# Kernel tuning notes

Measured on AMD Instinct MI355X. Metric: run time of the kernel, lower is better.

Reference implementation:

```python
import jax, jax.numpy as jnp
import numpy as np

N, H, W, C = 8, 64, 64, 256  # C//4 = 64 query channels, HW = 4096 attention size


def setup_inputs() -> dict:
    key = jax.random.key(0)
    k1, k2, k3, k4 = jax.random.split(key, 4)
    src_mask = jax.random.uniform(k1, (N, H, W), dtype=jnp.float32)
    src_feature = jax.random.normal(k2, (N, H, W, C), dtype=jnp.float32)
    ref_feature = jax.random.normal(k3, (N, H, W, C), dtype=jnp.float32)
    w_query = jax.random.normal(k4, (C, C // 4), dtype=jnp.float32) * 0.02  # 1x1 conv weight
    return {"src_mask": src_mask, "src_feature": src_feature,
            "ref_feature": ref_feature, "w_query": w_query}


def _apply_attention_map(att_map, features):
    n, h, w, c = features.shape
    pixels = features.reshape(n, h * w, c).transpose(0, 2, 1)  # (N, C, HW)
    att_out = jnp.einsum('ncp,npq->ncq', pixels, att_map)      # (N, C, HW)
    return att_out.reshape(n, h, w, c)


def reference(src_mask, src_feature, ref_feature, w_query):
    n, h, w, c = src_feature.shape
    # 1x1 conv (no bias): per-pixel channel projection C -> C//4
    query = jnp.einsum('nhwc,cd->nhwd', src_feature, w_query).reshape(n, h * w, -1)
    # full (HW x HW) attention map, softmax over keys
    att_map = jax.nn.softmax(jnp.einsum('npd,nqd->npq', query, query), axis=-1)
    # original module applies the map to src_feature twice (src_att and ref_att)
    att_out = _apply_attention_map(att_map, src_feature)
    src_att = att_out
    ref_att = att_out
    m = src_mask[..., None]  # (N, H, W, 1)
    ex_guide_flow = m * ref_att + (1.0 - m) * ref_feature
    return jnp.concatenate([ex_guide_flow, src_att], axis=-1)  # (N, H, W, 2C)
```

## Files before the change

### kernel.cpp

```cpp
#include <hip/hip_runtime.h>

typedef unsigned short u16;
typedef unsigned int u32;
typedef __attribute__((ext_vector_type(8))) __bf16 bf16x8;
typedef __attribute__((ext_vector_type(8))) _Float16 f16x8;
typedef __attribute__((ext_vector_type(4))) float f32x4;

__device__ __forceinline__ float b2f(u16 b) {
    union { u32 u; float f; } v; v.u = ((u32)b) << 16; return v.f;
}
__device__ __forceinline__ u16 f2bf(float f) {
    union { float f; u32 u; } v; v.f = f;
    u32 u = v.u;
    return (u16)((u + 0x7fffu + ((u >> 16) & 1u)) >> 16);
}
__device__ __forceinline__ u16 f2h(float f) {
    _Float16 h = (_Float16)f;
    return __builtin_bit_cast(u16, h);
}
__device__ __forceinline__ bf16x8 ldg8b(const u16* p) {
    uint4 v = *(const uint4*)p;
    return __builtin_bit_cast(bf16x8, v);
}
__device__ __forceinline__ f16x8 ldg8h(const u16* p) {
    uint4 v = *(const uint4*)p;
    return __builtin_bit_cast(f16x8, v);
}
__device__ __forceinline__ f32x4 mfma_bf(bf16x8 a, bf16x8 b, f32x4 c) {
    return __builtin_amdgcn_mfma_f32_16x16x32_bf16(a, b, c, 0, 0, 0);
}
__device__ __forceinline__ f32x4 mfma_h(f16x8 a, f16x8 b, f32x4 c) {
    return __builtin_amdgcn_mfma_f32_16x16x32_f16(a, b, c, 0, 0, 0);
}
__device__ __forceinline__ void gld16(const u16* g, u16* l) {
    __builtin_amdgcn_global_load_lds(
        (const __attribute__((address_space(1))) u32*)g,
        (__attribute__((address_space(3))) u32*)l, 16, 0, 0);
}


__global__ void k0_wt(const float* __restrict__ Wq,
                      u16* __restrict__ Wthi, u16* __restrict__ Wtlo) {
    int idx = blockIdx.x * 256 + threadIdx.x;
    int c = idx >> 6, d = idx & 63;
    float w = Wq[idx];
    u16 hi = f2bf(w);
    float rem = w - b2f(hi);
    Wthi[d * 256 + c] = hi;
    Wtlo[d * 256 + c] = f2bf(rem);
}

__global__ __launch_bounds__(256) void k1_query(
    const float* __restrict__ F, const u16* __restrict__ Wthi,
    const u16* __restrict__ Wtlo, u16* __restrict__ Qh) {
    const int t = threadIdx.x;
    const int w = t >> 6, L = t & 63, lane16 = L & 15, quad = L >> 4;
    const int R0 = blockIdx.x * 64;
    const int row = R0 + w * 16 + lane16;
    const f32x4 z4 = {0.f, 0.f, 0.f, 0.f};
    f32x4 acc[4] = {z4, z4, z4, z4};
    union U8 { bf16x8 v; u16 s[8]; };
#pragma unroll
    for (int ks = 0; ks < 8; ++ks) {
        const float* fp = F + (size_t)row * 256 + ks * 32 + quad * 8;
        float4 x0 = *(const float4*)fp;
        float4 x1 = *(const float4*)(fp + 4);
        float xs[8] = {x0.x, x0.y, x0.z, x0.w, x1.x, x1.y, x1.z, x1.w};
        U8 ahi, alo;
#pragma unroll
        for (int j = 0; j < 8; ++j) {
            u16 h = f2bf(xs[j]);
            ahi.s[j] = h;
            alo.s[j] = f2bf(xs[j] - b2f(h));
        }
#pragma unroll
        for (int nt = 0; nt < 4; ++nt) {
            const int off = (nt * 16 + lane16) * 256 + ks * 32 + quad * 8;
            bf16x8 bh = ldg8b(Wthi + off);
            bf16x8 bl = ldg8b(Wtlo + off);
            acc[nt] = mfma_bf(ahi.v, bh, acc[nt]);
            acc[nt] = mfma_bf(alo.v, bh, acc[nt]);
            acc[nt] = mfma_bf(ahi.v, bl, acc[nt]);
        }
    }
    const int orow = R0 + w * 16 + quad * 4;
#pragma unroll
    for (int nt = 0; nt < 4; ++nt) {
        const int d = nt * 16 + lane16;
#pragma unroll
        for (int r = 0; r < 4; ++r) {
            const int p = orow + r;
            Qh[(size_t)p * 64 + (d ^ ((p & 7) << 3))] = f2h(acc[nt][r]);
        }
    }
}

__global__ __launch_bounds__(256) void k2_suminv(
    const u16* __restrict__ Q, float* __restrict__ inv_l) {
    const int t = threadIdx.x;
    const int w = t >> 6, L = t & 63, lane16 = L & 15, quad = L >> 4, l7 = lane16 & 7;
    const int bx = blockIdx.x;
    const int n = bx & 7, pb = bx >> 3;
    const int P0 = pb * 32;
    const u16* Qn = Q + (size_t)n * 4096 * 64;

    f16x8 ap[2][2];
#pragma unroll
    for (int st = 0; st < 2; ++st) {
        const int row = P0 + st * 16 + lane16;
        ap[st][0] = ldg8h(Qn + row * 64 + ((quad * 8) ^ (l7 * 8)));
        ap[st][1] = ldg8h(Qn + row * 64 + ((32 + quad * 8) ^ (l7 * 8)));
    }
    float sums[2][4];
#pragma unroll
    for (int st = 0; st < 2; ++st)
#pragma unroll
        for (int r = 0; r < 4; ++r) sums[st][r] = 0.f;

    const f32x4 z4 = {0.f, 0.f, 0.f, 0.f};
    for (int s = 0; s < 32; ++s) {
#pragma unroll
        for (int nt = 0; nt < 2; ++nt) {
            const int qr = w * 1024 + s * 32 + nt * 16 + lane16;
            f16x8 b0 = ldg8h(Qn + qr * 64 + ((quad * 8) ^ (l7 * 8)));
            f16x8 b1 = ldg8h(Qn + qr * 64 + ((32 + quad * 8) ^ (l7 * 8)));
#pragma unroll
            for (int st = 0; st < 2; ++st) {
                f32x4 z = z4;
                z = mfma_h(ap[st][0], b0, z);
                z = mfma_h(ap[st][1], b1, z);
                sums[st][0] += __expf(z[0]);
                sums[st][1] += __expf(z[1]);
                sums[st][2] += __expf(z[2]);
                sums[st][3] += __expf(z[3]);
            }
        }
    }
    __shared__ float red[4][32];
#pragma unroll
    for (int st = 0; st < 2; ++st)
#pragma unroll
        for (int r = 0; r < 4; ++r) {
            float v = sums[st][r];
            v += __shfl_xor(v, 1);
            v += __shfl_xor(v, 2);
            v += __shfl_xor(v, 4);
            v += __shfl_xor(v, 8);
            if (lane16 == 0) red[w][st * 16 + quad * 4 + r] = v;
        }
    __syncthreads();
    if (t < 32) {
        float tot = red[0][t] + red[1][t] + red[2][t] + red[3][t];
        inv_l[n * 4096 + P0 + t] = 1.0f / tot;
    }
}

__global__ __launch_bounds__(256) void k3_gt(
    const float* __restrict__ F, u16* __restrict__ Gt) {
    const int t = threadIdx.x;
    const int bx = blockIdx.x;
    const int n = bx >> 6, s = bx & 63;
    const int p0 = s * 64;
    __shared__ float tile[64][65];
    const float* Fn = F + (size_t)n * 4096 * 256;
    u16* Gn = Gt + (size_t)(n * 64 + s) * 16384;
#pragma unroll 1
    for (int ct = 0; ct < 4; ++ct) {
        const int c0 = ct * 64;
        if (ct > 0) __syncthreads();
#pragma unroll
        for (int k = 0; k < 16; ++k) {
            int idx = k * 256 + t;
            int r = idx >> 6, cc = idx & 63;
            tile[r][cc] = Fn[(size_t)(p0 + r) * 256 + c0 + cc];
        }
        __syncthreads();
#pragma unroll
        for (int k = 0; k < 2; ++k) {
            int u = k * 256 + t;
            int cc = u & 63, S = u >> 6;
            int G = S ^ (cc & 7);
            u16 v[8];
#pragma unroll
            for (int j = 0; j < 8; ++j) v[j] = f2bf(tile[G * 8 + j][cc]);
            uint4 pk;
            pk.x = (u32)v[0] | ((u32)v[1] << 16);
            pk.y = (u32)v[2] | ((u32)v[3] << 16);
            pk.z = (u32)v[4] | ((u32)v[5] << 16);
            pk.w = (u32)v[6] | ((u32)v[7] << 16);
            *(uint4*)&Gn[(c0 + cc) * 64 + S * 8] = pk;
        }
    }
}

__global__ __launch_bounds__(256, 2) void k4_attn(
    const u16* __restrict__ Q, const u16* __restrict__ Gt,
    const float* __restrict__ invl, const float* __restrict__ mask,
    const float* __restrict__ ref, float* __restrict__ out) {
    const int t = threadIdx.x;
    const int w = t >> 6, L = t & 63, lane16 = L & 15, quad = L >> 4, l7 = lane16 & 7;
    const int bx = blockIdx.x;
    const int n = bx & 7, qb = bx >> 3;
    const int q0 = qb << 6;

    __shared__ u16 sGt[16384];
    __shared__ u16 sQp[4096];
    __shared__ u16 sP[4096];

    const u16* Qn = Q + (size_t)n * 4096 * 64;
    const u16* Gtn = Gt + (size_t)n * 64 * 16384;
    const float* iln = invl + n * 4096;

    f16x8 bq[4][2];
#pragma unroll
    for (int qt = 0; qt < 4; ++qt) {
        const int row = q0 + qt * 16 + lane16;
        bq[qt][0] = ldg8h(Qn + row * 64 + ((quad * 8) ^ (l7 * 8)));
        bq[qt][1] = ldg8h(Qn + row * 64 + ((32 + quad * 8) ^ (l7 * 8)));
    }

    const int pl = w * 16 + lane16;
    const int sA0 = pl * 64 + ((quad * 8) ^ (l7 * 8));
    const int sA1 = pl * 64 + ((32 + quad * 8) ^ (l7 * 8));
    int wrP[4];
#pragma unroll
    for (int qt = 0; qt < 4; ++qt)
        wrP[qt] = (qt * 16 + lane16) * 64 +
                  ((w * 16 + 8 * (quad >> 1)) ^ (l7 * 8)) + 4 * (quad & 1);
    const int dl = L * 8;

    const f32x4 z4 = {0.f, 0.f, 0.f, 0.f};
    f32x4 acc[4][4];
#pragma unroll
    for (int a = 0; a < 4; ++a)
#pragma unroll
        for (int b = 0; b < 4; ++b) acc[a][b] = z4;

#pragma unroll
    for (int j = 0; j < 2; ++j) {
        const int c = w * 2 + j;
        gld16(Qn + c * 512 + dl, &sQp[c * 512]);
    }
    __syncthreads();

#pragma unroll 1
    for (int i = 0; i < 64; ++i) {
#pragma unroll
        for (int j = 0; j < 8; ++j) {
            const int c = w * 8 + j;
            gld16(Gtn + (size_t)i * 16384 + c * 512 + dl, &sGt[c * 512]);
        }
        {
            f16x8 a0 = ldg8h(&sQp[sA0]);
            f16x8 a1 = ldg8h(&sQp[sA1]);
            float4 il4 = *(const float4*)(iln + i * 64 + w * 16 + quad * 4);
#pragma unroll
            for (int qt = 0; qt < 4; ++qt) {
                f32x4 z = z4;
                z = mfma_h(a0, bq[qt][0], z);
                z = mfma_h(a1, bq[qt][1], z);
                ushort4 pk;
                pk.x = f2bf(__expf(z[0]) * il4.x);
                pk.y = f2bf(__expf(z[1]) * il4.y);
                pk.z = f2bf(__expf(z[2]) * il4.z);
                pk.w = f2bf(__expf(z[3]) * il4.w);
                *(ushort4*)&sP[wrP[qt]] = pk;
            }
        }
        __syncthreads();
        if (i + 1 < 64) {
#pragma unroll
            for (int j = 0; j < 2; ++j) {
                const int c = w * 2 + j;
                gld16(Qn + (size_t)(i + 1) * 4096 + c * 512 + dl, &sQp[c * 512]);
            }
        }
#pragma unroll
        for (int h = 0; h < 2; ++h) {
            bf16x8 af[4], bb[4];
#pragma unroll
            for (int m = 0; m < 4; ++m)
                af[m] = ldg8b(&sP[(m * 16 + lane16) * 64 + ((h * 32 + quad * 8) ^ (l7 * 8))]);
#pragma unroll
            for (int nt = 0; nt < 4; ++nt)
                bb[nt] = ldg8b(&sGt[(w * 64 + nt * 16 + lane16) * 64 +
                                    ((h * 32 + quad * 8) ^ (l7 * 8))]);
#pragma unroll
            for (int nt = 0; nt < 4; ++nt)
#pragma unroll
                for (int m = 0; m < 4; ++m)
                    acc[m][nt] = mfma_bf(af[m], bb[nt], acc[m][nt]);
        }
        __syncthreads();
    }

    const int tb = qb >> 2;
    const int cb = (qb & 3) * 64;
    const float* maskn = mask + n * 4096;
    const float* refn = ref + (size_t)n * 4096 * 256;
    float* outn = out + (size_t)n * 4096 * 512;
#pragma unroll
    for (int nt = 0; nt < 4; ++nt) {
        const int ch = w * 64 + nt * 16 + lane16;
        const int pixel = ch * 16 + tb;
        const float m = maskn[pixel];
#pragma unroll
        for (int mt = 0; mt < 4; ++mt) {
            const int c4 = cb + mt * 16 + quad * 4;
            float4 r4 = *(const float4*)(refn + (size_t)pixel * 256 + c4);
            float a0 = acc[mt][nt][0], a1 = acc[mt][nt][1];
            float a2 = acc[mt][nt][2], a3 = acc[mt][nt][3];
            float4 a4 = {a0, a1, a2, a3};
            float4 bl4 = {m * a0 + (1.f - m) * r4.x,
                          m * a1 + (1.f - m) * r4.y,
                          m * a2 + (1.f - m) * r4.z,
                          m * a3 + (1.f - m) * r4.w};
            *(float4*)(outn + (size_t)pixel * 512 + 256 + c4) = a4;
            *(float4*)(outn + (size_t)pixel * 512 + c4) = bl4;
        }
    }
}

extern "C" void kernel_launch(void* const* d_in, const int* in_sizes, int n_in,
                              void* d_out, int out_size, void* d_ws, size_t ws_size,
                              hipStream_t stream) {
    const float* mask = (const float*)d_in[0];
    const float* F    = (const float*)d_in[1];
    const float* ref  = (const float*)d_in[2];
    const float* Wq   = (const float*)d_in[3];
    float* out = (float*)d_out;
    char* ws = (char*)d_ws;

    u16*   Wthi = (u16*)ws;
    u16*   Wtlo = (u16*)(ws + 32768);
    u16*   Qh   = (u16*)(ws + 65536);
    float* invl = (float*)(ws + 65536 + 4194304);
    u16*   Gt   = (u16*)(ws + 65536 + 4194304 + 131072);

    k0_wt    <<<64,   256, 0, stream>>>(Wq, Wthi, Wtlo);
    k1_query <<<512,  256, 0, stream>>>(F, Wthi, Wtlo, Qh);
    k2_suminv<<<1024, 256, 0, stream>>>(Qh, invl);
    k3_gt    <<<512,  256, 0, stream>>>(F, Gt);
    k4_attn  <<<512,  256, 0, stream>>>(Qh, Gt, invl, mask, ref, out);
}
```

Baseline: 271.7 us.

## Double-buffer P tile, read Gt and Q directly from global, fold normalizer into exp2

The attention kernel no longer stages the Gt value tile and Q slice in LDS through async global-to-LDS loads. MFMA operands are now read straight from global memory, and the P tile is double-buffered so the next step's softmax probabilities are computed while the current step's product runs, leaving one barrier per iteration instead of two. The row-sum kernel now stores -log2(sum), and each probability becomes exp2(z*log2e + lg), replacing an exp and a multiply with an fma and an exp2, with packed bf16 conversion. The risk is that Gt is re-read from global/L2 by every wave instead of being shared through LDS, adding memory traffic and latency.

```diff
diff --git a/kernel.cpp b/kernel.cpp
--- a/kernel.cpp
+++ b/kernel.cpp
@@ -18,6 +18,11 @@
     _Float16 h = (_Float16)f;
     return __builtin_bit_cast(u16, h);
 }
+__device__ __forceinline__ u32 pkbf2(float a, float b) {
+    u16 x = __builtin_bit_cast(u16, (__bf16)a);
+    u16 y = __builtin_bit_cast(u16, (__bf16)b);
+    return (u32)x | ((u32)y << 16);
+}
 __device__ __forceinline__ bf16x8 ldg8b(const u16* p) {
     uint4 v = *(const uint4*)p;
     return __builtin_bit_cast(bf16x8, v);
@@ -32,11 +37,8 @@
 __device__ __forceinline__ f32x4 mfma_h(f16x8 a, f16x8 b, f32x4 c) {
     return __builtin_amdgcn_mfma_f32_16x16x32_f16(a, b, c, 0, 0, 0);
 }
-__device__ __forceinline__ void gld16(const u16* g, u16* l) {
-    __builtin_amdgcn_global_load_lds(
-        (const __attribute__((address_space(1))) u32*)g,
-        (__attribute__((address_space(3))) u32*)l, 16, 0, 0);
-}
+
+#define LOG2E 1.44269504088896340736f
 
 
 __global__ void k0_wt(const float* __restrict__ Wq,
@@ -96,7 +98,7 @@
 }
 
 __global__ __launch_bounds__(256) void k2_suminv(
-    const u16* __restrict__ Q, float* __restrict__ inv_l) {
+    const u16* __restrict__ Q, float* __restrict__ lgl) {
     const int t = threadIdx.x;
     const int w = t >> 6, L = t & 63, lane16 = L & 15, quad = L >> 4, l7 = lane16 & 7;
     const int bx = blockIdx.x;
@@ -151,7 +153,7 @@
     __syncthreads();
     if (t < 32) {
         float tot = red[0][t] + red[1][t] + red[2][t] + red[3][t];
-        inv_l[n * 4096 + P0 + t] = 1.0f / tot;
+        lgl[n * 4096 + P0 + t] = -__log2f(tot);
     }
 }
 
@@ -195,7 +197,7 @@
 
 __global__ __launch_bounds__(256, 2) void k4_attn(
     const u16* __restrict__ Q, const u16* __restrict__ Gt,
-    const float* __restrict__ invl, const float* __restrict__ mask,
+    const float* __restrict__ lgl, const float* __restrict__ mask,
     const float* __restrict__ ref, float* __restrict__ out) {
     const int t = threadIdx.x;
     const int w = t >> 6, L = t & 63, lane16 = L & 15, quad = L >> 4, l7 = lane16 & 7;
@@ -203,13 +205,11 @@
     const int n = bx & 7, qb = bx >> 3;
     const int q0 = qb << 6;
 
-    __shared__ u16 sGt[16384];
-    __shared__ u16 sQp[4096];
-    __shared__ u16 sP[4096];
+    __shared__ u16 sP[2][4096];
 
     const u16* Qn = Q + (size_t)n * 4096 * 64;
     const u16* Gtn = Gt + (size_t)n * 64 * 16384;
-    const float* iln = invl + n * 4096;
+    const float* iln = lgl + n * 4096;
 
     f16x8 bq[4][2];
 #pragma unroll
@@ -219,15 +219,24 @@
         bq[qt][1] = ldg8h(Qn + row * 64 + ((32 + quad * 8) ^ (l7 * 8)));
     }
 
-    const int pl = w * 16 + lane16;
-    const int sA0 = pl * 64 + ((quad * 8) ^ (l7 * 8));
-    const int sA1 = pl * 64 + ((32 + quad * 8) ^ (l7 * 8));
+    const int sAg0 = (w * 16 + lane16) * 64 + ((quad * 8) ^ (l7 * 8));
+    const int sAg1 = (w * 16 + lane16) * 64 + ((32 + quad * 8) ^ (l7 * 8));
     int wrP[4];
 #pragma unroll
     for (int qt = 0; qt < 4; ++qt)
         wrP[qt] = (qt * 16 + lane16) * 64 +
                   ((w * 16 + 8 * (quad >> 1)) ^ (l7 * 8)) + 4 * (quad & 1);
-    const int dl = L * 8;
+    int rdP[4][2], gOf[4][2];
+#pragma unroll
+    for (int m = 0; m < 4; ++m)
+#pragma unroll
+        for (int h = 0; h < 2; ++h)
+            rdP[m][h] = (m * 16 + lane16) * 64 + ((h * 32 + quad * 8) ^ (l7 * 8));
+#pragma unroll
+    for (int nt = 0; nt < 4; ++nt)
+#pragma unroll
+        for (int h = 0; h < 2; ++h)
+            gOf[nt][h] = (w * 64 + nt * 16 + lane16) * 64 + ((h * 32 + quad * 8) ^ (l7 * 8));
 
     const f32x4 z4 = {0.f, 0.f, 0.f, 0.f};
     f32x4 acc[4][4];
@@ -236,60 +245,61 @@
 #pragma unroll
         for (int b = 0; b < 4; ++b) acc[a][b] = z4;
 
-#pragma unroll
-    for (int j = 0; j < 2; ++j) {
-        const int c = w * 2 + j;
-        gld16(Qn + c * 512 + dl, &sQp[c * 512]);
+    {
+        f16x8 a0 = ldg8h(Qn + sAg0);
+        f16x8 a1 = ldg8h(Qn + sAg1);
+        float4 il4 = *(const float4*)(iln + w * 16 + quad * 4);
+        float lg[4] = {il4.x, il4.y, il4.z, il4.w};
+#pragma unroll
+        for (int qt = 0; qt < 4; ++qt) {
+            f32x4 z = z4;
+            z = mfma_h(a0, bq[qt][0], z);
+            z = mfma_h(a1, bq[qt][1], z);
+            uint2 pk;
+            pk.x = pkbf2(__builtin_exp2f(__builtin_fmaf(z[0], LOG2E, lg[0])),
+                         __builtin_exp2f(__builtin_fmaf(z[1], LOG2E, lg[1])));
+            pk.y = pkbf2(__builtin_exp2f(__builtin_fmaf(z[2], LOG2E, lg[2])),
+                         __builtin_exp2f(__builtin_fmaf(z[3], LOG2E, lg[3])));
+            *(uint2*)&sP[0][wrP[qt]] = pk;
+        }
     }
     __syncthreads();
 
 #pragma unroll 1
     for (int i = 0; i < 64; ++i) {
-#pragma unroll
-        for (int j = 0; j < 8; ++j) {
-            const int c = w * 8 + j;
-            gld16(Gtn + (size_t)i * 16384 + c * 512 + dl, &sGt[c * 512]);
-        }
-        {
-            f16x8 a0 = ldg8h(&sQp[sA0]);
-            f16x8 a1 = ldg8h(&sQp[sA1]);
-            float4 il4 = *(const float4*)(iln + i * 64 + w * 16 + quad * 4);
+        const u16* sPc = &sP[i & 1][0];
+        u16* sPn = &sP[(i + 1) & 1][0];
+        const u16* gstep = Gtn + (size_t)i * 16384;
+#pragma unroll
+        for (int h = 0; h < 2; ++h) {
+            bf16x8 af[4], bb[4];
+#pragma unroll
+            for (int m = 0; m < 4; ++m) af[m] = ldg8b(&sPc[rdP[m][h]]);
+#pragma unroll
+            for (int nt = 0; nt < 4; ++nt) bb[nt] = ldg8b(gstep + gOf[nt][h]);
+#pragma unroll
+            for (int nt = 0; nt < 4; ++nt)
+#pragma unroll
+                for (int m = 0; m < 4; ++m)
+                    acc[m][nt] = mfma_bf(af[m], bb[nt], acc[m][nt]);
+        }
+        if (i + 1 < 64) {
+            f16x8 a0 = ldg8h(Qn + (i + 1) * 4096 + sAg0);
+            f16x8 a1 = ldg8h(Qn + (i + 1) * 4096 + sAg1);
+            float4 il4 = *(const float4*)(iln + (i + 1) * 64 + w * 16 + quad * 4);
+            float lg[4] = {il4.x, il4.y, il4.z, il4.w};
 #pragma unroll
             for (int qt = 0; qt < 4; ++qt) {
                 f32x4 z = z4;
                 z = mfma_h(a0, bq[qt][0], z);
                 z = mfma_h(a1, bq[qt][1], z);
-                ushort4 pk;
-                pk.x = f2bf(__expf(z[0]) * il4.x);
-                pk.y = f2bf(__expf(z[1]) * il4.y);
-                pk.z = f2bf(__expf(z[2]) * il4.z);
-                pk.w = f2bf(__expf(z[3]) * il4.w);
-                *(ushort4*)&sP[wrP[qt]] = pk;
+                uint2 pk;
+                pk.x = pkbf2(__builtin_exp2f(__builtin_fmaf(z[0], LOG2E, lg[0])),
+                             __builtin_exp2f(__builtin_fmaf(z[1], LOG2E, lg[1])));
+                pk.y = pkbf2(__builtin_exp2f(__builtin_fmaf(z[2], LOG2E, lg[2])),
+                             __builtin_exp2f(__builtin_fmaf(z[3], LOG2E, lg[3])));
+                *(uint2*)&sPn[wrP[qt]] = pk;
             }
-        }
-        __syncthreads();
-        if (i + 1 < 64) {
-#pragma unroll
-            for (int j = 0; j < 2; ++j) {
-                const int c = w * 2 + j;
-                gld16(Qn + (size_t)(i + 1) * 4096 + c * 512 + dl, &sQp[c * 512]);
-            }
-        }
-#pragma unroll
-        for (int h = 0; h < 2; ++h) {
-            bf16x8 af[4], bb[4];
-#pragma unroll
-            for (int m = 0; m < 4; ++m)
-                af[m] = ldg8b(&sP[(m * 16 + lane16) * 64 + ((h * 32 + quad * 8) ^ (l7 * 8))]);
-#pragma unroll
-            for (int nt = 0; nt < 4; ++nt)
-                bb[nt] = ldg8b(&sGt[(w * 64 + nt * 16 + lane16) * 64 +
-                                    ((h * 32 + quad * 8) ^ (l7 * 8))]);
-#pragma unroll
-            for (int nt = 0; nt < 4; ++nt)
-#pragma unroll
-                for (int m = 0; m < 4; ++m)
-                    acc[m][nt] = mfma_bf(af[m], bb[nt], acc[m][nt]);
         }
         __syncthreads();
     }
@@ -334,12 +344,12 @@
     u16*   Wthi = (u16*)ws;
     u16*   Wtlo = (u16*)(ws + 32768);
     u16*   Qh   = (u16*)(ws + 65536);
-    float* invl = (float*)(ws + 65536 + 4194304);
+    float* lgl  = (float*)(ws + 65536 + 4194304);
     u16*   Gt   = (u16*)(ws + 65536 + 4194304 + 131072);
 
     k0_wt    <<<64,   256, 0, stream>>>(Wq, Wthi, Wtlo);
     k1_query <<<512,  256, 0, stream>>>(F, Wthi, Wtlo, Qh);
-    k2_suminv<<<1024, 256, 0, stream>>>(Qh, invl);
+    k2_suminv<<<1024, 256, 0, stream>>>(Qh, lgl);
     k3_gt    <<<512,  256, 0, stream>>>(F, Gt);
-    k4_attn  <<<512,  256, 0, stream>>>(Qh, Gt, invl, mask, ref, out);
-}
+    k4_attn  <<<512,  256, 0, stream>>>(Qh, Gt, lgl, mask, ref, out);
+}
```

Measured after the change: 335.5 us. +23.5%, slower.

## Use 8 waves in attention kernel, fold normalizer into exp2, use hardware bf16 conversion

Applied to the files above, without the earlier changes.

The attention kernel now launches 512 threads per block (8 waves), halving per-wave channel tiles and query tiles so each wave holds fewer accumulators. The aim is to raise occupancy and hide the latency of the LDS and global loads. The row-sum kernel now stores -log2 of the sum, so the probability becomes a single fma plus exp2 instead of exp and a multiply. Float-to-bf16 conversion now uses the compiler's native __bf16 cast, which can map to a packed hardware convert. More waves share each barrier, so synchronization costs more, and the pre-scaled exp2 form may change rounding slightly.

```diff
diff --git a/kernel.cpp b/kernel.cpp
--- a/kernel.cpp
+++ b/kernel.cpp
@@ -10,13 +10,16 @@
     union { u32 u; float f; } v; v.u = ((u32)b) << 16; return v.f;
 }
 __device__ __forceinline__ u16 f2bf(float f) {
-    union { float f; u32 u; } v; v.f = f;
-    u32 u = v.u;
-    return (u16)((u + 0x7fffu + ((u >> 16) & 1u)) >> 16);
+    return __builtin_bit_cast(u16, (__bf16)f);
 }
 __device__ __forceinline__ u16 f2h(float f) {
     _Float16 h = (_Float16)f;
     return __builtin_bit_cast(u16, h);
+}
+__device__ __forceinline__ u32 pkbf2(float a, float b) {
+    u16 x = __builtin_bit_cast(u16, (__bf16)a);
+    u16 y = __builtin_bit_cast(u16, (__bf16)b);
+    return (u32)x | ((u32)y << 16);
 }
 __device__ __forceinline__ bf16x8 ldg8b(const u16* p) {
     uint4 v = *(const uint4*)p;
@@ -37,6 +40,8 @@
         (const __attribute__((address_space(1))) u32*)g,
         (__attribute__((address_space(3))) u32*)l, 16, 0, 0);
 }
+
+#define LOG2E 1.44269504088896340736f
 
 
 __global__ void k0_wt(const float* __restrict__ Wq,
@@ -96,7 +101,7 @@
 }
 
 __global__ __launch_bounds__(256) void k2_suminv(
-    const u16* __restrict__ Q, float* __restrict__ inv_l) {
+    const u16* __restrict__ Q, float* __restrict__ lgl) {
     const int t = threadIdx.x;
     const int w = t >> 6, L = t & 63, lane16 = L & 15, quad = L >> 4, l7 = lane16 & 7;
     const int bx = blockIdx.x;
@@ -151,7 +156,7 @@
     __syncthreads();
     if (t < 32) {
         float tot = red[0][t] + red[1][t] + red[2][t] + red[3][t];
-        inv_l[n * 4096 + P0 + t] = 1.0f / tot;
+        lgl[n * 4096 + P0 + t] = -__log2f(tot);
     }
 }
 
@@ -180,28 +185,27 @@
             int u = k * 256 + t;
             int cc = u & 63, S = u >> 6;
             int G = S ^ (cc & 7);
-            u16 v[8];
-#pragma unroll
-            for (int j = 0; j < 8; ++j) v[j] = f2bf(tile[G * 8 + j][cc]);
             uint4 pk;
-            pk.x = (u32)v[0] | ((u32)v[1] << 16);
-            pk.y = (u32)v[2] | ((u32)v[3] << 16);
-            pk.z = (u32)v[4] | ((u32)v[5] << 16);
-            pk.w = (u32)v[6] | ((u32)v[7] << 16);
+            pk.x = pkbf2(tile[G * 8 + 0][cc], tile[G * 8 + 1][cc]);
+            pk.y = pkbf2(tile[G * 8 + 2][cc], tile[G * 8 + 3][cc]);
+            pk.z = pkbf2(tile[G * 8 + 4][cc], tile[G * 8 + 5][cc]);
+            pk.w = pkbf2(tile[G * 8 + 6][cc], tile[G * 8 + 7][cc]);
             *(uint4*)&Gn[(c0 + cc) * 64 + S * 8] = pk;
         }
     }
 }
 
-__global__ __launch_bounds__(256, 2) void k4_attn(
+__global__ __launch_bounds__(512, 4) void k4_attn(
     const u16* __restrict__ Q, const u16* __restrict__ Gt,
-    const float* __restrict__ invl, const float* __restrict__ mask,
+    const float* __restrict__ lgl, const float* __restrict__ mask,
     const float* __restrict__ ref, float* __restrict__ out) {
     const int t = threadIdx.x;
     const int w = t >> 6, L = t & 63, lane16 = L & 15, quad = L >> 4, l7 = lane16 & 7;
     const int bx = blockIdx.x;
     const int n = bx & 7, qb = bx >> 3;
     const int q0 = qb << 6;
+    const int ps = w & 3;
+    const int qh = w >> 2;
 
     __shared__ u16 sGt[16384];
     __shared__ u16 sQp[4096];
@@ -209,84 +213,77 @@
 
     const u16* Qn = Q + (size_t)n * 4096 * 64;
     const u16* Gtn = Gt + (size_t)n * 64 * 16384;
-    const float* iln = invl + n * 4096;
-
-    f16x8 bq[4][2];
-#pragma unroll
-    for (int qt = 0; qt < 4; ++qt) {
-        const int row = q0 + qt * 16 + lane16;
+    const float* iln = lgl + n * 4096;
+
+    f16x8 bq[2][2];
+#pragma unroll
+    for (int qt = 0; qt < 2; ++qt) {
+        const int row = q0 + qh * 32 + qt * 16 + lane16;
         bq[qt][0] = ldg8h(Qn + row * 64 + ((quad * 8) ^ (l7 * 8)));
         bq[qt][1] = ldg8h(Qn + row * 64 + ((32 + quad * 8) ^ (l7 * 8)));
     }
 
-    const int pl = w * 16 + lane16;
+    const int pl = ps * 16 + lane16;
     const int sA0 = pl * 64 + ((quad * 8) ^ (l7 * 8));
     const int sA1 = pl * 64 + ((32 + quad * 8) ^ (l7 * 8));
-    int wrP[4];
-#pragma unroll
-    for (int qt = 0; qt < 4; ++qt)
-        wrP[qt] = (qt * 16 + lane16) * 64 +
-                  ((w * 16 + 8 * (quad >> 1)) ^ (l7 * 8)) + 4 * (quad & 1);
+    int wrP[2];
+#pragma unroll
+    for (int qt = 0; qt < 2; ++qt)
+        wrP[qt] = (qh * 32 + qt * 16 + lane16) * 64 +
+                  ((ps * 16 + 8 * (quad >> 1)) ^ (l7 * 8)) + 4 * (quad & 1);
     const int dl = L * 8;
 
     const f32x4 z4 = {0.f, 0.f, 0.f, 0.f};
-    f32x4 acc[4][4];
+    f32x4 acc[4][2];
 #pragma unroll
     for (int a = 0; a < 4; ++a)
 #pragma unroll
-        for (int b = 0; b < 4; ++b) acc[a][b] = z4;
-
-#pragma unroll
-    for (int j = 0; j < 2; ++j) {
-        const int c = w * 2 + j;
-        gld16(Qn + c * 512 + dl, &sQp[c * 512]);
-    }
+        for (int b = 0; b < 2; ++b) acc[a][b] = z4;
+
+    gld16(Qn + w * 512 + dl, &sQp[w * 512]);
     __syncthreads();
 
 #pragma unroll 1
     for (int i = 0; i < 64; ++i) {
 #pragma unroll
-        for (int j = 0; j < 8; ++j) {
-            const int c = w * 8 + j;
+        for (int j = 0; j < 4; ++j) {
+            const int c = w * 4 + j;
             gld16(Gtn + (size_t)i * 16384 + c * 512 + dl, &sGt[c * 512]);
         }
         {
             f16x8 a0 = ldg8h(&sQp[sA0]);
             f16x8 a1 = ldg8h(&sQp[sA1]);
-            float4 il4 = *(const float4*)(iln + i * 64 + w * 16 + quad * 4);
-#pragma unroll
-            for (int qt = 0; qt < 4; ++qt) {
+            float4 il4 = *(const float4*)(iln + i * 64 + ps * 16 + quad * 4);
+            float lg0 = il4.x, lg1 = il4.y, lg2 = il4.z, lg3 = il4.w;
+#pragma unroll
+            for (int qt = 0; qt < 2; ++qt) {
                 f32x4 z = z4;
                 z = mfma_h(a0, bq[qt][0], z);
                 z = mfma_h(a1, bq[qt][1], z);
-                ushort4 pk;
-                pk.x = f2bf(__expf(z[0]) * il4.x);
-                pk.y = f2bf(__expf(z[1]) * il4.y);
-                pk.z = f2bf(__expf(z[2]) * il4.z);
-                pk.w = f2bf(__expf(z[3]) * il4.w);
-                *(ushort4*)&sP[wrP[qt]] = pk;
+                uint2 pk;
+                pk.x = pkbf2(__builtin_exp2f(__builtin_fmaf(z[0], LOG2E, lg0)),
+                             __builtin_exp2f(__builtin_fmaf(z[1], LOG2E, lg1)));
+                pk.y = pkbf2(__builtin_exp2f(__builtin_fmaf(z[2], LOG2E, lg2)),
+                             __builtin_exp2f(__builtin_fmaf(z[3], LOG2E, lg3)));
+                *(uint2*)&sP[wrP[qt]] = pk;
             }
         }
         __syncthreads();
         if (i + 1 < 64) {
-#pragma unroll
-            for (int j = 0; j < 2; ++j) {
-                const int c = w * 2 + j;
-                gld16(Qn + (size_t)(i + 1) * 4096 + c * 512 + dl, &sQp[c * 512]);
-            }
+            gld16(Qn + (size_t)(i + 1) * 4096 + w * 512 + dl, &sQp[w * 512]);
         }
 #pragma unroll
         for (int h = 0; h < 2; ++h) {
-            bf16x8 af[4], bb[4];
+            bf16x8 af[4], bb[2];
 #pragma unroll
             for (int m = 0; m < 4; ++m)
                 af[m] = ldg8b(&sP[(m * 16 + lane16) * 64 + ((h * 32 + quad * 8) ^ (l7 * 8))]);
 #pragma unroll
-            for (int nt = 0; nt < 4; ++nt)
-                bb[nt] = ldg8b(&sGt[(w * 64 + nt * 16 + lane16) * 64 +
+            for (int nt = 0; nt < 2; ++nt)
+                bb[nt] = ldg8b(&sGt[(w * 32 + nt * 16 + lane16) * 64 +
                                     ((h * 32 + quad * 8) ^ (l7 * 8))]);
 #pragma unroll
-            for (int nt = 0; nt < 4; ++nt)
+            for (int nt = 0; nt < 2; ++nt)
 #pragma unroll
                 for (int m = 0; m < 4; ++m)
                     acc[m][nt] = mfma_bf(af[m], bb[nt], acc[m][nt]);
@@ -300,8 +297,8 @@
     const float* refn = ref + (size_t)n * 4096 * 256;
     float* outn = out + (size_t)n * 4096 * 512;
 #pragma unroll
-    for (int nt = 0; nt < 4; ++nt) {
-        const int ch = w * 64 + nt * 16 + lane16;
+    for (int nt = 0; nt < 2; ++nt) {
+        const int ch = w * 32 + nt * 16 + lane16;
         const int pixel = ch * 16 + tb;
         const float m = maskn[pixel];
 #pragma unroll
@@ -334,12 +331,12 @@
     u16*   Wthi = (u16*)ws;
     u16*   Wtlo = (u16*)(ws + 32768);
     u16*   Qh   = (u16*)(ws + 65536);
-    float* invl = (float*)(ws + 65536 + 4194304);
+    float* lgl  = (float*)(ws + 65536 + 4194304);
     u16*   Gt   = (u16*)(ws + 65536 + 4194304 + 131072);
 
     k0_wt    <<<64,   256, 0, stream>>>(Wq, Wthi, Wtlo);
     k1_query <<<512,  256, 0, stream>>>(F, Wthi, Wtlo, Qh);
-    k2_suminv<<<1024, 256, 0, stream>>>(Qh, invl);
+    k2_suminv<<<1024, 256, 0, stream>>>(Qh, lgl);
     k3_gt    <<<512,  256, 0, stream>>>(F, Gt);
-    k4_attn  <<<512,  256, 0, stream>>>(Qh, Gt, invl, mask, ref, out);
-}
+    k4_attn  <<<512,  512, 0, stream>>>(Qh, Gt, lgl, mask, ref, out);
+}
```

New measurement: 294.9 us. 8.6% more time.

## Fuse query projection and bf16 transpose of features into one kernel

Applied to the files above, without the earlier changes.

Merges the query projection kernel and the feature transpose/convert kernel so the fp32 feature tile is read from global memory once into LDS and reused for both the Gt layout write and the split-bf16 MFMA projection. This removes one full pass over the 32 MB feature tensor and one kernel launch. It also swaps the manual rounding in the transpose path for native bf16 conversion, and pads the tile to 68 columns so the float4 reads from LDS are aligned, which may add bank conflicts on the column-wise transpose reads.

```diff
diff --git a/kernel.cpp b/kernel.cpp
--- a/kernel.cpp
+++ b/kernel.cpp
@@ -17,6 +17,11 @@
 __device__ __forceinline__ u16 f2h(float f) {
     _Float16 h = (_Float16)f;
     return __builtin_bit_cast(u16, h);
+}
+__device__ __forceinline__ u32 pkbf2(float a, float b) {
+    u16 x = __builtin_bit_cast(u16, (__bf16)a);
+    u16 y = __builtin_bit_cast(u16, (__bf16)b);
+    return (u32)x | ((u32)y << 16);
 }
 __device__ __forceinline__ bf16x8 ldg8b(const u16* p) {
     uint4 v = *(const uint4*)p;
@@ -50,37 +55,70 @@
     Wtlo[d * 256 + c] = f2bf(rem);
 }
 
-__global__ __launch_bounds__(256) void k1_query(
+__global__ __launch_bounds__(256) void k13_query_gt(
     const float* __restrict__ F, const u16* __restrict__ Wthi,
-    const u16* __restrict__ Wtlo, u16* __restrict__ Qh) {
+    const u16* __restrict__ Wtlo, u16* __restrict__ Qh,
+    u16* __restrict__ Gt) {
     const int t = threadIdx.x;
     const int w = t >> 6, L = t & 63, lane16 = L & 15, quad = L >> 4;
-    const int R0 = blockIdx.x * 64;
-    const int row = R0 + w * 16 + lane16;
+    const int bx = blockIdx.x;
+    const int R0 = bx * 64;
+    const int n = bx >> 6, s = bx & 63;
+
+    __shared__ float tile[64][68];
+    const float* Fn = F + (size_t)R0 * 256;
+    u16* Gn = Gt + (size_t)(n * 64 + s) * 16384;
+
     const f32x4 z4 = {0.f, 0.f, 0.f, 0.f};
     f32x4 acc[4] = {z4, z4, z4, z4};
     union U8 { bf16x8 v; u16 s[8]; };
-#pragma unroll
-    for (int ks = 0; ks < 8; ++ks) {
-        const float* fp = F + (size_t)row * 256 + ks * 32 + quad * 8;
-        float4 x0 = *(const float4*)fp;
-        float4 x1 = *(const float4*)(fp + 4);
-        float xs[8] = {x0.x, x0.y, x0.z, x0.w, x1.x, x1.y, x1.z, x1.w};
-        U8 ahi, alo;
-#pragma unroll
-        for (int j = 0; j < 8; ++j) {
-            u16 h = f2bf(xs[j]);
-            ahi.s[j] = h;
-            alo.s[j] = f2bf(xs[j] - b2f(h));
-        }
-#pragma unroll
-        for (int nt = 0; nt < 4; ++nt) {
-            const int off = (nt * 16 + lane16) * 256 + ks * 32 + quad * 8;
-            bf16x8 bh = ldg8b(Wthi + off);
-            bf16x8 bl = ldg8b(Wtlo + off);
-            acc[nt] = mfma_bf(ahi.v, bh, acc[nt]);
-            acc[nt] = mfma_bf(alo.v, bh, acc[nt]);
-            acc[nt] = mfma_bf(ahi.v, bl, acc[nt]);
+
+#pragma unroll 1
+    for (int ct = 0; ct < 4; ++ct) {
+        const int c0 = ct * 64;
+        if (ct > 0) __syncthreads();
+#pragma unroll
+        for (int k = 0; k < 16; ++k) {
+            int idx = k * 256 + t;
+            int r = idx >> 6, cc = idx & 63;
+            tile[r][cc] = Fn[(size_t)r * 256 + c0 + cc];
+        }
+        __syncthreads();
+#pragma unroll
+        for (int k = 0; k < 2; ++k) {
+            int u = k * 256 + t;
+            int cc = u & 63, S = u >> 6;
+            int G = S ^ (cc & 7);
+            uint4 pk;
+            pk.x = pkbf2(tile[G * 8 + 0][cc], tile[G * 8 + 1][cc]);
+            pk.y = pkbf2(tile[G * 8 + 2][cc], tile[G * 8 + 3][cc]);
+            pk.z = pkbf2(tile[G * 8 + 4][cc], tile[G * 8 + 5][cc]);
+            pk.w = pkbf2(tile[G * 8 + 6][cc], tile[G * 8 + 7][cc]);
+            *(uint4*)&Gn[(c0 + cc) * 64 + S * 8] = pk;
+        }
+#pragma unroll
+        for (int kk = 0; kk < 2; ++kk) {
+            const int ks = ct * 2 + kk;
+            const float* tp = &tile[w * 16 + lane16][kk * 32 + quad * 8];
+            float4 x0 = *(const float4*)tp;
+            float4 x1 = *(const float4*)(tp + 4);
+            float xs[8] = {x0.x, x0.y, x0.z, x0.w, x1.x, x1.y, x1.z, x1.w};
+            U8 ahi, alo;
+#pragma unroll
+            for (int j = 0; j < 8; ++j) {
+                u16 h = f2bf(xs[j]);
+                ahi.s[j] = h;
+                alo.s[j] = f2bf(xs[j] - b2f(h));
+            }
+#pragma unroll
+            for (int nt = 0; nt < 4; ++nt) {
+                const int off = (nt * 16 + lane16) * 256 + ks * 32 + quad * 8;
+                bf16x8 bh = ldg8b(Wthi + off);
+                bf16x8 bl = ldg8b(Wtlo + off);
+                acc[nt] = mfma_bf(ahi.v, bh, acc[nt]);
+                acc[nt] = mfma_bf(alo.v, bh, acc[nt]);
+                acc[nt] = mfma_bf(ahi.v, bl, acc[nt]);
+            }
         }
     }
     const int orow = R0 + w * 16 + quad * 4;
@@ -152,44 +190,6 @@
     if (t < 32) {
         float tot = red[0][t] + red[1][t] + red[2][t] + red[3][t];
         inv_l[n * 4096 + P0 + t] = 1.0f / tot;
-    }
-}
-
-__global__ __launch_bounds__(256) void k3_gt(
-    const float* __restrict__ F, u16* __restrict__ Gt) {
-    const int t = threadIdx.x;
-    const int bx = blockIdx.x;
-    const int n = bx >> 6, s = bx & 63;
-    const int p0 = s * 64;
-    __shared__ float tile[64][65];
-    const float* Fn = F + (size_t)n * 4096 * 256;
-    u16* Gn = Gt + (size_t)(n * 64 + s) * 16384;
-#pragma unroll 1
-    for (int ct = 0; ct < 4; ++ct) {
-        const int c0 = ct * 64;
-        if (ct > 0) __syncthreads();
-#pragma unroll
-        for (int k = 0; k < 16; ++k) {
-            int idx = k * 256 + t;
-            int r = idx >> 6, cc = idx & 63;
-            tile[r][cc] = Fn[(size_t)(p0 + r) * 256 + c0 + cc];
-        }
-        __syncthreads();
-#pragma unroll
-        for (int k = 0; k < 2; ++k) {
-            int u = k * 256 + t;
-            int cc = u & 63, S = u >> 6;
-            int G = S ^ (cc & 7);
-            u16 v[8];
-#pragma unroll
-            for (int j = 0; j < 8; ++j) v[j] = f2bf(tile[G * 8 + j][cc]);
-            uint4 pk;
-            pk.x = (u32)v[0] | ((u32)v[1] << 16);
-            pk.y = (u32)v[2] | ((u32)v[3] << 16);
-            pk.z = (u32)v[4] | ((u32)v[5] << 16);
-            pk.w = (u32)v[6] | ((u32)v[7] << 16);
-            *(uint4*)&Gn[(c0 + cc) * 64 + S * 8] = pk;
-        }
     }
 }
 
@@ -337,9 +337,8 @@
     float* invl = (float*)(ws + 65536 + 4194304);
     u16*   Gt   = (u16*)(ws + 65536 + 4194304 + 131072);
 
-    k0_wt    <<<64,   256, 0, stream>>>(Wq, Wthi, Wtlo);
-    k1_query <<<512,  256, 0, stream>>>(F, Wthi, Wtlo, Qh);
-    k2_suminv<<<1024, 256, 0, stream>>>(Qh, invl);
-    k3_gt    <<<512,  256, 0, stream>>>(F, Gt);
-    k4_attn  <<<512,  256, 0, stream>>>(Qh, Gt, invl, mask, ref, out);
-}
+    k0_wt        <<<64,   256, 0, stream>>>(Wq, Wthi, Wtlo);
+    k13_query_gt <<<512,  256, 0, stream>>>(F, Wthi, Wtlo, Qh, Gt);
+    k2_suminv    <<<1024, 256, 0, stream>>>(Qh, invl);
+    k4_attn      <<<512,  256, 0, stream>>>(Qh, Gt, invl, mask, ref, out);
+}
```

Result: no change. 268.1 us (-1.3%).
